# Optimization experiments

Measured on AMD Instinct MI355X. Metric: run time of the kernel, lower is better.

The kernel has to match this reference:

```python
import jax, jax.numpy as jnp
import numpy as np

B, L, R, D = 64, 512, 512, 512
F_CONV, H = 100, 60

def setup_inputs() -> dict:
    key = jax.random.key(0)
    ks = jax.random.split(key, 8)
    l_lengths = jax.random.randint(ks[0], (B,), L // 2, L + 1)
    r_lengths = jax.random.randint(ks[1], (B,), R // 2, R + 1)
    l_vectors = jax.random.normal(ks[2], (L, B, D), jnp.float32)
    r_vectors = jax.random.normal(ks[3], (R, B, D), jnp.float32)
    Wconv = jax.random.normal(ks[4], (F_CONV, D), jnp.float32) / np.sqrt(D).astype(np.float32)
    bconv = jnp.zeros((F_CONV,), jnp.float32)
    Wd = jax.random.normal(ks[5], (H, 2 * F_CONV), jnp.float32) / np.sqrt(2 * F_CONV).astype(np.float32)
    bd = jnp.zeros((H,), jnp.float32)
    return {"l_lengths": l_lengths, "l_vectors": l_vectors, "r_lengths": r_lengths,
            "r_vectors": r_vectors, "Wconv": Wconv, "bconv": bconv, "Wd": Wd, "bd": bd}

def reference(l_lengths, l_vectors, r_lengths, r_vectors, Wconv, bconv, Wd, bd):
    Lm, Bm, Dm = l_vectors.shape
    Rm = r_vectors.shape[0]
    # masks, seq-first [L,B] like pad_sequence output
    l_mask = (jnp.arange(Lm)[:, None] < l_lengths[None, :]).astype(l_vectors.dtype)
    r_mask = (jnp.arange(Rm)[:, None] < r_lengths[None, :]).astype(r_vectors.dtype)
    lmT, rmT = l_mask.T, r_mask.T  # [B,L], [B,R]

    # co-attention scores [B,L,R]
    attention = jnp.einsum('lbd,rbd->blr', l_vectors, r_vectors)
    attention = attention * lmT[:, :, None] * rmT[:, None, :]

    att_r = jax.nn.softmax(attention - 10.0 * (1.0 - lmT[:, :, None]), axis=1)
    att_r = att_r * lmT[:, :, None]
    att_r = att_r / (att_r.sum(axis=1, keepdims=True) + 1e-13)

    att_l = jax.nn.softmax(attention - 10.0 * (1.0 - rmT[:, None, :]), axis=2)
    att_l = att_l * rmT[:, None, :]
    att_l = att_l / (att_l.sum(axis=2, keepdims=True) + 1e-13)

    # ---- left side: stats + top-1 hard attention ----
    rl = r_lengths.astype(l_vectors.dtype)[:, None]
    l_mean = att_l.sum(axis=2) / rl                              # [B,L]
    l_w = (att_l * att_l).sum(axis=2) / rl - l_mean * l_mean
    l_w = l_w / jnp.maximum(l_mean, 0.001)
    l_a = att_l.max(axis=2)                                      # top-1 value [B,L]
    l_i = att_l.argmax(axis=2)                                   # top-1 index [B,L]
    l_i = l_i * lmT.astype(l_i.dtype)
    l_a = l_a / jnp.maximum(l_a, 0.001)                          # k=1: sum == value
    gathered = jnp.take_along_axis(r_vectors, l_i.T[:, :, None], axis=0)  # [L,B,D]
    l_counter = l_a.T[:, :, None] * gathered
    l_c = l_w.T[:, :, None] * jnp.abs(l_vectors - l_counter) * l_mask[:, :, None]

    # ---- right side ----
    ll = l_lengths.astype(r_vectors.dtype)[:, None]
    r_mean = att_r.sum(axis=1) / ll                              # [B,R]
    r_w = (att_r * att_r).sum(axis=1) / ll - r_mean * r_mean
    r_w = r_w / jnp.maximum(r_mean, 0.001)
    r_a = att_r.max(axis=1)                                      # [B,R]
    r_i = att_r.argmax(axis=1)
    r_i = r_i * rmT.astype(r_i.dtype)
    r_a = r_a / jnp.maximum(r_a, 0.001)
    gathered_r = jnp.take_along_axis(l_vectors, r_i.T[:, :, None], axis=0)  # [R,B,D]
    r_counter = r_a.T[:, :, None] * gathered_r
    r_c = r_w.T[:, :, None] * jnp.abs(r_vectors - r_counter) * r_mask[:, :, None]

    # SentenceConv(1, 100, dim): kernel (1, dim) conv == per-position linear,
    # ReLU, masked max-pool over the sequence.
    def sconv(x, mask):  # x [S,B,D], mask [S,B]
        h = jax.nn.relu(jnp.einsum('sbd,fd->bsf', x, Wconv) + bconv)  # [B,S,F]
        h = h - (1.0 - mask.T)[:, :, None] * 1e9
        return h.max(axis=1)  # [B,F]

    feats = jnp.concatenate([sconv(l_c, l_mask), sconv(r_c, r_mask)], axis=1)  # [B,200]
    return jax.nn.relu(feats @ Wd.T + bd)  # [B,60]
```

## Files before the change

kernel.cpp:

```cpp
#include <hip/hip_runtime.h>
#include <math.h>

#define BB 64
#define LL 512
#define RR 512
#define DD 512
#define FC 100
#define FP 112
#define HH 60
#define BD (BB*DD)

typedef __attribute__((ext_vector_type(8))) short bf16x8;
typedef __attribute__((ext_vector_type(4))) float f32x4;

__device__ __forceinline__ unsigned short bf16rne(float x) {
  unsigned u = __float_as_uint(x);
  return (unsigned short)((u + 0x7fffu + ((u >> 16) & 1u)) >> 16);
}
__device__ __forceinline__ float bf16tof(unsigned short h) {
  return __uint_as_float((unsigned)h << 16);
}

__device__ __forceinline__ void bar_lgkm() {
  asm volatile("s_waitcnt lgkmcnt(0)" ::: "memory");
  __builtin_amdgcn_s_barrier();
}

__device__ __forceinline__ void split2(float x0, float x1, unsigned& h2, unsigned& l2) {
  unsigned u0 = __float_as_uint(x0), u1 = __float_as_uint(x1);
  h2 = __builtin_amdgcn_perm(u1, u0, 0x07060302u);
  float r0 = x0 - __uint_as_float(u0 & 0xffff0000u);
  float r1 = x1 - __uint_as_float(u1 & 0xffff0000u);
  l2 = __builtin_amdgcn_perm(__float_as_uint(r1), __float_as_uint(r0), 0x07060302u);
}

template <int N>
__device__ __forceinline__ float ror_max_f(float v) {
  return fmaxf(v, __uint_as_float(__builtin_amdgcn_mov_dpp(__float_as_uint(v), 0x120 | N, 0xf, 0xf, true)));
}
template <int N>
__device__ __forceinline__ float ror_add_f(float v) {
  return v + __uint_as_float(__builtin_amdgcn_mov_dpp(__float_as_uint(v), 0x120 | N, 0xf, 0xf, true));
}
template <int N>
__device__ __forceinline__ int ror_min_i(int v) {
  int o = __builtin_amdgcn_mov_dpp(v, 0x120 | N, 0xf, 0xf, true);
  return o < v ? o : v;
}
__device__ __forceinline__ float row16_max(float v) {
  v = ror_max_f<1>(v); v = ror_max_f<2>(v); v = ror_max_f<4>(v); return ror_max_f<8>(v);
}
__device__ __forceinline__ float row16_sum(float v) {
  v = ror_add_f<1>(v); v = ror_add_f<2>(v); v = ror_add_f<4>(v); return ror_add_f<8>(v);
}
__device__ __forceinline__ int row16_min(int v) {
  v = ror_min_i<1>(v); v = ror_min_i<2>(v); v = ror_min_i<4>(v); return ror_min_i<8>(v);
}

__global__ __launch_bounds__(512, 2) void gemm_att(const float* __restrict__ lv,
                                                   const float* __restrict__ rv,
                                                   const int* __restrict__ llen,
                                                   const int* __restrict__ rlen,
                                                   float4* __restrict__ lpart,
                                                   float4* __restrict__ rpart) {
  __shared__ __align__(16) unsigned short Ah[2][256][32];
  __shared__ __align__(16) unsigned short Al[2][256][32];
  __shared__ __align__(16) unsigned short Bh[2][256][32];
  __shared__ __align__(16) unsigned short Bl[2][256][32];

  const int bid = blockIdx.x;
  const int wid = (bid & 7) * 32 + (bid >> 3);
  const int b  = wid >> 2;
  const int l0 = ((wid >> 1) & 1) * 256;
  const int r0 = (wid & 1) * 256;

  const int t = threadIdx.x;
  const int srow = t >> 1;
  const int half = t & 1;

  const float* Abase = lv + (size_t)(l0 + srow) * BD + b * DD + half * 16;
  const float* Bbase = rv + (size_t)(r0 + srow) * BD + b * DD + half * 16;

  const int sl0 = (((2 * half) ^ ((srow >> 1) & 3)) * 8);
  const int sl1 = (((2 * half + 1) ^ ((srow >> 1) & 3)) * 8);

  const int lane = t & 63;
  const int wv = t >> 6;
  const int wrow = wv >> 2;
  const int wcol = wv & 3;
  const int fr = lane & 15;
  const int kh = lane >> 4;
  const int koff = (kh ^ ((fr >> 1) & 3)) * 8;

  float4 pa[4], pb[4];

#define LOADCHUNK(n) { const int cn_ = ((n) < 15 ? (n) : 15) * 32; \
    const float* An = Abase + cn_; const float* Bn = Bbase + cn_; \
    pa[0] = *(const float4*)(An);     pa[1] = *(const float4*)(An + 4); \
    pa[2] = *(const float4*)(An + 8); pa[3] = *(const float4*)(An + 12); \
    pb[0] = *(const float4*)(Bn);     pb[1] = *(const float4*)(Bn + 4); \
    pb[2] = *(const float4*)(Bn + 8); pb[3] = *(const float4*)(Bn + 12); }

#define STAGE(nb) { unsigned h01, l01, h23, l23, h45, l45, h67, l67; \
    split2(pa[0].x, pa[0].y, h01, l01); split2(pa[0].z, pa[0].w, h23, l23); \
    split2(pa[1].x, pa[1].y, h45, l45); split2(pa[1].z, pa[1].w, h67, l67); \
    *(uint4*)&Ah[nb][srow][sl0] = make_uint4(h01, h23, h45, h67); \
    *(uint4*)&Al[nb][srow][sl0] = make_uint4(l01, l23, l45, l67); \
    split2(pa[2].x, pa[2].y, h01, l01); split2(pa[2].z, pa[2].w, h23, l23); \
    split2(pa[3].x, pa[3].y, h45, l45); split2(pa[3].z, pa[3].w, h67, l67); \
    *(uint4*)&Ah[nb][srow][sl1] = make_uint4(h01, h23, h45, h67); \
    *(uint4*)&Al[nb][srow][sl1] = make_uint4(l01, l23, l45, l67); \
    split2(pb[0].x, pb[0].y, h01, l01); split2(pb[0].z, pb[0].w, h23, l23); \
    split2(pb[1].x, pb[1].y, h45, l45); split2(pb[1].z, pb[1].w, h67, l67); \
    *(uint4*)&Bh[nb][srow][sl0] = make_uint4(h01, h23, h45, h67); \
    *(uint4*)&Bl[nb][srow][sl0] = make_uint4(l01, l23, l45, l67); \
    split2(pb[2].x, pb[2].y, h01, l01); split2(pb[2].z, pb[2].w, h23, l23); \
    split2(pb[3].x, pb[3].y, h45, l45); split2(pb[3].z, pb[3].w, h67, l67); \
    *(uint4*)&Bh[nb][srow][sl1] = make_uint4(h01, h23, h45, h67); \
    *(uint4*)&Bl[nb][srow][sl1] = make_uint4(l01, l23, l45, l67); }

#define COMPUTE(cb) { bf16x8 bh4[4], bl4[4]; \
    _Pragma("unroll") \
    for (int j = 0; j < 4; ++j) { \
      bh4[j] = *(const bf16x8*)&Bh[cb][wcol * 64 + j * 16 + fr][koff]; \
      bl4[j] = *(const bf16x8*)&Bl[cb][wcol * 64 + j * 16 + fr][koff]; \
    } \
    __builtin_amdgcn_s_setprio(1); \
    _Pragma("unroll") \
    for (int i = 0; i < 8; ++i) { \
      bf16x8 a_h = *(const bf16x8*)&Ah[cb][wrow * 128 + i * 16 + fr][koff]; \
      bf16x8 a_l = *(const bf16x8*)&Al[cb][wrow * 128 + i * 16 + fr][koff]; \
      _Pragma("unroll") \
      for (int j = 0; j < 4; ++j) { \
        acc[i][j] = __builtin_amdgcn_mfma_f32_16x16x32_bf16(a_h, bh4[j], acc[i][j], 0, 0, 0); \
        acc[i][j] = __builtin_amdgcn_mfma_f32_16x16x32_bf16(a_h, bl4[j], acc[i][j], 0, 0, 0); \
        acc[i][j] = __builtin_amdgcn_mfma_f32_16x16x32_bf16(a_l, bh4[j], acc[i][j], 0, 0, 0); \
      } \
    } \
    __builtin_amdgcn_s_setprio(0); }

  f32x4 acc[8][4];
#pragma unroll
  for (int i = 0; i < 8; ++i)
#pragma unroll
    for (int j = 0; j < 4; ++j) acc[i][j] = (f32x4){0.f, 0.f, 0.f, 0.f};

  LOADCHUNK(0);
  STAGE(0);
  LOADCHUNK(1);
  bar_lgkm();

  for (int p2 = 0; p2 < 8; ++p2) {
    const int c = p2 * 2;
    STAGE(1);
    LOADCHUNK(c + 2);
    COMPUTE(0);
    bar_lgkm();
    STAGE(0);
    LOADCHUNK(c + 3);
    COMPUTE(1);
    bar_lgkm();
  }

  const int ll_ = llen[b], rl_ = rlen[b];
  __syncthreads();
  float4* rowsc = (float4*)&Ah[0][0][0];
  float4* colsc = (float4*)&Bh[0][0][0];

  const int rbase = r0 + wcol * 64 + fr;
  bool vr4[4]; int rr4[4];
#pragma unroll
  for (int j = 0; j < 4; ++j) { rr4[j] = rbase + j * 16; vr4[j] = rr4[j] < rl_; }

#pragma unroll
  for (int i = 0; i < 8; ++i) {
#pragma unroll
    for (int q = 0; q < 4; ++q) {
      const int trow = wrow * 128 + i * 16 + kh * 4 + q;
      const bool vl = (l0 + trow) < ll_;
      float s[4];
      float M = -1e30f;
#pragma unroll
      for (int j = 0; j < 4; ++j) {
        float raw = acc[i][j][q];
        s[j] = !vr4[j] ? -10.f : (vl ? raw : 0.f);
        M = fmaxf(M, s[j]);
      }
      M = row16_max(M);
      float zv = 0.f, q2 = 0.f;
      int loc = 0x7fffffff;
#pragma unroll
      for (int j = 0; j < 4; ++j) {
        float e = __expf(s[j] - M);
        if (vr4[j]) {
          zv += e; q2 += e * e;
          if (s[j] == M && rr4[j] < loc) loc = rr4[j];
        }
      }
      zv = row16_sum(zv);
      q2 = row16_sum(q2);
      loc = row16_min(loc);
      if (fr == 0)
        rowsc[wcol * 256 + trow] = make_float4(M, zv, q2, __int_as_float(loc));
    }
  }

#pragma unroll
  for (int j = 0; j < 4; ++j) {
    const int tcol = wcol * 64 + j * 16 + fr;
    const bool vr = (r0 + tcol) < rl_;
    float M = -1e30f;
#pragma unroll
    for (int i = 0; i < 8; ++i)
#pragma unroll
      for (int q = 0; q < 4; ++q) {
        int lg = l0 + wrow * 128 + i * 16 + kh * 4 + q;
        bool vl = lg < ll_;
        float sv = !vl ? -10.f : (vr ? acc[i][j][q] : 0.f);
        M = fmaxf(M, sv);
      }
    M = fmaxf(M, __shfl_xor(M, 16, 64));
    M = fmaxf(M, __shfl_xor(M, 32, 64));
    float zv = 0.f, q2 = 0.f;
    int loc = 0x7fffffff;
#pragma unroll
    for (int i = 0; i < 8; ++i)
#pragma unroll
      for (int q = 0; q < 4; ++q) {
        int lg = l0 + wrow * 128 + i * 16 + kh * 4 + q;
        bool vl = lg < ll_;
        float sv = !vl ? -10.f : (vr ? acc[i][j][q] : 0.f);
        float e = __expf(sv - M);
        if (vl) {
          zv += e; q2 += e * e;
          if (sv == M && lg < loc) loc = lg;
        }
      }
    zv += __shfl_xor(zv, 16, 64); zv += __shfl_xor(zv, 32, 64);
    q2 += __shfl_xor(q2, 16, 64); q2 += __shfl_xor(q2, 32, 64);
    { int o = __shfl_xor(loc, 16, 64); loc = o < loc ? o : loc; }
    { int o = __shfl_xor(loc, 32, 64); loc = o < loc ? o : loc; }
    if (kh == 0)
      colsc[wrow * 256 + tcol] = make_float4(M, zv, q2, __int_as_float(loc));
  }

  __syncthreads();

  if (t < 256) {
    float4 p = rowsc[t];
    float M = p.x, zv = p.y, q2 = p.z;
    int loc = __float_as_int(p.w);
#pragma unroll
    for (int w2 = 1; w2 < 4; ++w2) {
      float4 o = rowsc[w2 * 256 + t];
      float M1 = o.x;
      float Mn = fmaxf(M, M1);
      float c0 = __expf(M - Mn), c1 = __expf(M1 - Mn);
      zv = zv * c0 + o.y * c1;
      q2 = q2 * c0 * c0 + o.z * c1 * c1;
      int loc1 = __float_as_int(o.w);
      loc = (M1 > M) ? loc1 : ((M1 == M && loc1 < loc) ? loc1 : loc);
      M = Mn;
    }
    lpart[((size_t)(b * 512 + l0 + t)) * 2 + (r0 >> 8)] =
        make_float4(M, zv, q2, __int_as_float(loc));
  } else {
    const int c = t - 256;
    float4 p = colsc[c];
    float M = p.x, zv = p.y, q2 = p.z;
    int loc = __float_as_int(p.w);
    {
      float4 o = colsc[256 + c];
      float M1 = o.x;
      float Mn = fmaxf(M, M1);
      float c0 = __expf(M - Mn), c1 = __expf(M1 - Mn);
      zv = zv * c0 + o.y * c1;
      q2 = q2 * c0 * c0 + o.z * c1 * c1;
      int loc1 = __float_as_int(o.w);
      loc = (M1 > M) ? loc1 : ((M1 == M && loc1 < loc) ? loc1 : loc);
      M = Mn;
    }
    rpart[((size_t)(b * 512 + r0 + c)) * 2 + (l0 >> 8)] =
        make_float4(M, zv, q2, __int_as_float(loc));
  }
#undef LOADCHUNK
#undef STAGE
#undef COMPUTE
}

__global__ __launch_bounds__(256) void stats_merge(const float4* __restrict__ lpart,
    const float4* __restrict__ rpart,
    const int* __restrict__ llen, const int* __restrict__ rlen,
    float* __restrict__ lwv, float* __restrict__ lan, int* __restrict__ lidx,
    float* __restrict__ rwv, float* __restrict__ ran, int* __restrict__ ridx) {
  const int gid = blockIdx.x * 256 + threadIdx.x;
  const int side = gid >> 15;
  const int pos = gid & 32767;
  const int b = pos >> 9, p = pos & 511;
  const float4* part = (side ? rpart : lpart) + (size_t)pos * 2;
  float4 P0 = part[0], P1 = part[1];
  float M = P0.x, zv = P0.y, q2 = P0.z;
  int loc = __float_as_int(P0.w);
  {
    float M1 = P1.x;
    float Mn = fmaxf(M, M1);
    float c0 = __expf(M - Mn), c1 = __expf(M1 - Mn);
    zv = zv * c0 + P1.y * c1;
    q2 = q2 * c0 * c0 + P1.z * c1 * c1;
    int loc1 = __float_as_int(P1.w);
    loc = (M1 > M) ? loc1 : ((M1 == M && loc1 < loc) ? loc1 : loc);
    M = Mn;
  }
  const int len = side ? llen[b] : rlen[b];
  const int own = side ? rlen[b] : llen[b];
  const int ninv = side ? (LL - llen[b]) : (RR - rlen[b]);
  float z0 = zv + (float)ninv * __expf(-10.f - M);
  float S = zv / z0;
  float inv = 1.f / (S + 1e-13f);
  float sumq = S * inv;
  float mean = sumq / (float)len;
  float sumq2 = q2 / (z0 * z0) * inv * inv;
  float var = sumq2 / (float)len - mean * mean;
  float wv = var / fmaxf(mean, 0.001f);
  float qmax = inv / z0;
  float an = qmax / fmaxf(qmax, 0.001f);
  int idx = (p < own && loc != 0x7fffffff) ? loc : 0;
  if (side == 0) { lwv[pos] = wv; lan[pos] = an; lidx[pos] = idx; }
  else           { rwv[pos] = wv; ran[pos] = an; ridx[pos] = idx; }
}

__global__ void prep_w(const float* __restrict__ Wconv,
                       unsigned short* __restrict__ Whg, unsigned short* __restrict__ Wlg) {
  int i = blockIdx.x * 256 + threadIdx.x;
  if (i < FP * DD) {
    int f = i >> 9;
    float w = (f < FC) ? Wconv[i] : 0.f;
    unsigned short h = bf16rne(w);
    unsigned short l = bf16rne(w - bf16tof(h));
    Whg[i] = h; Wlg[i] = l;
  }
}

__global__ __launch_bounds__(256) void conv_pool_mfma(const float* __restrict__ lv,
    const float* __restrict__ rv,
    const float* __restrict__ lwv, const float* __restrict__ lan, const int* __restrict__ lidx,
    const float* __restrict__ rwv, const float* __restrict__ ran, const int* __restrict__ ridx,
    const int* __restrict__ llen, const int* __restrict__ rlen,
    const unsigned short* __restrict__ Whg, const unsigned short* __restrict__ Wlg,
    const float* __restrict__ bconv, float* __restrict__ feat) {
  __shared__ __align__(16) unsigned short Ah[128][40];
  __shared__ __align__(16) unsigned short Al[128][40];
  __shared__ __align__(16) unsigned short Wh[FP][40];
  __shared__ __align__(16) unsigned short Wl[FP][40];
  __shared__ float pool[4][FP];
  __shared__ float ppw[128], ppa[128];
  __shared__ int   ppi[128], ppv[128];

  const int bid = blockIdx.x;
  const int wid = (bid & 7) * 64 + (bid >> 3);
  const int side = wid >> 8;
  const int b    = (wid >> 2) & 63;
  const int s0   = (wid & 3) * 128;

  const int t = threadIdx.x;
  const float* x; const float* y; const float* wb; const float* ab; const int* ib; int plen;
  if (side == 0) { x = lv; y = rv; wb = lwv; ab = lan; ib = lidx; plen = llen[b]; }
  else           { x = rv; y = lv; wb = rwv; ab = ran; ib = ridx; plen = rlen[b]; }

  if (t < 128) {
    int pos = s0 + t;
    ppw[t] = wb[b * 512 + pos];
    ppa[t] = ab[b * 512 + pos];
    ppi[t] = ib[b * 512 + pos];
    ppv[t] = (pos < plen) ? 1 : 0;
  }
  __syncthreads();

  const int pos  = t >> 1;
  const int half = t & 1;
  const float w_ = ppw[pos];
  const float a_ = ppa[pos];
  const int   yi = ppi[pos];
  const float* xp = x + (size_t)(s0 + pos) * BD + b * DD + half * 16;
  const float* yp = y + (size_t)yi * BD + b * DD + half * 16;

  float4 xv[4], yv[4];
#pragma unroll
  for (int q = 0; q < 4; ++q) {
    xv[q] = *(const float4*)(xp + q * 4);
    yv[q] = *(const float4*)(yp + q * 4);
  }

  const int lane = t & 63;
  const int wvi = t >> 6;
  const int m0 = wvi * 32;
  const int fr = lane & 15;
  const int kh = lane >> 4;

  f32x4 acc[2][7];
#pragma unroll
  for (int i = 0; i < 2; ++i)
#pragma unroll
    for (int j = 0; j < 7; ++j) acc[i][j] = (f32x4){0.f, 0.f, 0.f, 0.f};

  for (int it = 0; it < 16; ++it) {
    const int k0 = it * 32;
    __syncthreads();
#pragma unroll
    for (int q = 0; q < 2; ++q) {
      float d0 = w_ * fabsf(xv[2*q].x   - a_ * yv[2*q].x);
      float d1 = w_ * fabsf(xv[2*q].y   - a_ * yv[2*q].y);
      float d2 = w_ * fabsf(xv[2*q].z   - a_ * yv[2*q].z);
      float d3 = w_ * fabsf(xv[2*q].w   - a_ * yv[2*q].w);
      float d4 = w_ * fabsf(xv[2*q+1].x - a_ * yv[2*q+1].x);
      float d5 = w_ * fabsf(xv[2*q+1].y - a_ * yv[2*q+1].y);
      float d6 = w_ * fabsf(xv[2*q+1].z - a_ * yv[2*q+1].z);
      float d7 = w_ * fabsf(xv[2*q+1].w - a_ * yv[2*q+1].w);
      unsigned h01, l01, h23, l23, h45, l45, h67, l67;
      split2(d0, d1, h01, l01);
      split2(d2, d3, h23, l23);
      split2(d4, d5, h45, l45);
      split2(d6, d7, h67, l67);
      *(uint4*)&Ah[pos][half * 16 + q * 8] = make_uint4(h01, h23, h45, h67);
      *(uint4*)&Al[pos][half * 16 + q * 8] = make_uint4(l01, l23, l45, l67);
    }
#pragma unroll
    for (int rep = 0; rep < 2; ++rep) {
      int idx = t + rep * 256;
      if (idx < FP * 4) {
        int f = idx >> 2, q = idx & 3;
        *(ulonglong2*)&Wh[f][q * 8] = *(const ulonglong2*)&Whg[f * DD + k0 + q * 8];
        *(ulonglong2*)&Wl[f][q * 8] = *(const ulonglong2*)&Wlg[f * DD + k0 + q * 8];
      }
    }
    if (it < 15) {
      const float* xn = xp + k0 + 32;
      const float* yn = yp + k0 + 32;
#pragma unroll
      for (int q = 0; q < 4; ++q) {
        xv[q] = *(const float4*)(xn + q * 4);
        yv[q] = *(const float4*)(yn + q * 4);
      }
    }
    __syncthreads();

    bf16x8 ah[2], al[2];
#pragma unroll
    for (int i = 0; i < 2; ++i) {
      ah[i] = *(const bf16x8*)&Ah[m0 + i * 16 + fr][kh * 8];
      al[i] = *(const bf16x8*)&Al[m0 + i * 16 + fr][kh * 8];
    }
#pragma unroll
    for (int j = 0; j < 7; ++j) {
      bf16x8 bh = *(const bf16x8*)&Wh[j * 16 + fr][kh * 8];
      bf16x8 bl = *(const bf16x8*)&Wl[j * 16 + fr][kh * 8];
#pragma unroll
      for (int i = 0; i < 2; ++i) {
        acc[i][j] = __builtin_amdgcn_mfma_f32_16x16x32_bf16(ah[i], bh, acc[i][j], 0, 0, 0);
        acc[i][j] = __builtin_amdgcn_mfma_f32_16x16x32_bf16(ah[i], bl, acc[i][j], 0, 0, 0);
        acc[i][j] = __builtin_amdgcn_mfma_f32_16x16x32_bf16(al[i], bh, acc[i][j], 0, 0, 0);
      }
    }
  }

#pragma unroll
  for (int j = 0; j < 7; ++j) {
    int f = j * 16 + fr;
    float bcv = (f < FC) ? bconv[f] : 0.f;
    float vmax = -1e30f;
#pragma unroll
    for (int i = 0; i < 2; ++i) {
#pragma unroll
      for (int q = 0; q < 4; ++q) {
        int sl = m0 + i * 16 + kh * 4 + q;
        if (ppv[sl]) vmax = fmaxf(vmax, fmaxf(acc[i][j][q] + bcv, 0.f));
      }
    }
    vmax = fmaxf(vmax, __shfl_xor(vmax, 16, 64));
    vmax = fmaxf(vmax, __shfl_xor(vmax, 32, 64));
    if (lane < 16) pool[wvi][f] = vmax;
  }
  __syncthreads();
  if (t < FC) {
    float v = fmaxf(fmaxf(pool[0][t], pool[1][t]), fmaxf(pool[2][t], pool[3][t]));
    if (v > -1e29f) atomicMax((int*)&feat[b * 200 + side * FC + t], __float_as_int(v));
  }
}

__global__ void dense_out(const float* __restrict__ feat, const float* __restrict__ Wd,
                          const float* __restrict__ bd, float* __restrict__ out) {
  int b = blockIdx.x, h = threadIdx.x;
  if (h < HH) {
    float s = bd[h];
    const float* fb = feat + b * 200;
    const float* wr = Wd + h * 200;
    for (int k = 0; k < 200; ++k) s += fb[k] * wr[k];
    out[b * HH + h] = fmaxf(s, 0.f);
  }
}

extern "C" void kernel_launch(void* const* d_in, const int* in_sizes, int n_in,
                              void* d_out, int out_size, void* d_ws, size_t ws_size,
                              hipStream_t stream) {
  (void)in_sizes; (void)n_in; (void)out_size; (void)ws_size;
  const int*   llen  = (const int*)d_in[0];
  const float* lv    = (const float*)d_in[1];
  const int*   rlen  = (const int*)d_in[2];
  const float* rv    = (const float*)d_in[3];
  const float* Wconv = (const float*)d_in[4];
  const float* bconv = (const float*)d_in[5];
  const float* Wd    = (const float*)d_in[6];
  const float* bd    = (const float*)d_in[7];
  float* out = (float*)d_out;
  char* ws = (char*)d_ws;
  size_t off = 0;
  unsigned short* Whg = (unsigned short*)(ws + off); off += (size_t)FP * DD * 2;
  unsigned short* Wlg = (unsigned short*)(ws + off); off += (size_t)FP * DD * 2;
  float4* lpart = (float4*)(ws + off); off += (size_t)BB * LL * 2 * 16;
  float4* rpart = (float4*)(ws + off); off += (size_t)BB * RR * 2 * 16;
  float* lwv = (float*)(ws + off); off += (size_t)BB * LL * 4;
  float* lan = (float*)(ws + off); off += (size_t)BB * LL * 4;
  int*   lidx= (int*)  (ws + off); off += (size_t)BB * LL * 4;
  float* rwv = (float*)(ws + off); off += (size_t)BB * RR * 4;
  float* ran = (float*)(ws + off); off += (size_t)BB * RR * 4;
  int*   ridx= (int*)  (ws + off); off += (size_t)BB * RR * 4;
  float* feat= (float*)(ws + off); off += (size_t)BB * 200 * 4;

  hipMemsetAsync(feat, 0, BB * 200 * 4, stream);
  prep_w<<<(FP * DD + 255) / 256, 256, 0, stream>>>(Wconv, Whg, Wlg);
  gemm_att<<<dim3(256), 512, 0, stream>>>(lv, rv, llen, rlen, lpart, rpart);
  stats_merge<<<dim3(256), 256, 0, stream>>>(lpart, rpart, llen, rlen,
                                             lwv, lan, lidx, rwv, ran, ridx);
  conv_pool_mfma<<<dim3(512), 256, 0, stream>>>(lv, rv, lwv, lan, lidx,
                                                rwv, ran, ridx, llen, rlen,
                                                Whg, Wlg, bconv, feat);
  dense_out<<<BB, 64, 0, stream>>>(feat, Wd, bd, out);
}
```

Measured before the change: 115.3 us.

## Double-buffer LDS tiles in conv_pool_mfma with XOR swizzle and one barrier per step

The conv/pool MFMA kernel is restructured to double-buffer its A and W tiles in shared memory. The next tile is staged while the current one is multiplied, so each k-step needs a single barrier instead of two. The padded 40-wide rows become 32-wide rows with an XOR swizzle to avoid bank conflicts, and s_setprio raises priority around the MFMA block. Launch bounds now request 2 blocks per CU. The risks are higher register pressure, the correctness of the custom bar_lgkm barrier, and the redundant final-iteration loads that are clamped to tile 15.

```diff
diff --git a/kernel.cpp b/kernel.cpp
--- a/kernel.cpp
+++ b/kernel.cpp
@@ -341,17 +341,17 @@
   }
 }
 
-__global__ __launch_bounds__(256) void conv_pool_mfma(const float* __restrict__ lv,
+__global__ __launch_bounds__(256, 2) void conv_pool_mfma(const float* __restrict__ lv,
     const float* __restrict__ rv,
     const float* __restrict__ lwv, const float* __restrict__ lan, const int* __restrict__ lidx,
     const float* __restrict__ rwv, const float* __restrict__ ran, const int* __restrict__ ridx,
     const int* __restrict__ llen, const int* __restrict__ rlen,
     const unsigned short* __restrict__ Whg, const unsigned short* __restrict__ Wlg,
     const float* __restrict__ bconv, float* __restrict__ feat) {
-  __shared__ __align__(16) unsigned short Ah[128][40];
-  __shared__ __align__(16) unsigned short Al[128][40];
-  __shared__ __align__(16) unsigned short Wh[FP][40];
-  __shared__ __align__(16) unsigned short Wl[FP][40];
+  __shared__ __align__(16) unsigned short Ah[2][128][32];
+  __shared__ __align__(16) unsigned short Al[2][128][32];
+  __shared__ __align__(16) unsigned short Wh[2][FP][32];
+  __shared__ __align__(16) unsigned short Wl[2][FP][32];
   __shared__ float pool[4][FP];
   __shared__ float ppw[128], ppa[128];
   __shared__ int   ppi[128], ppv[128];
@@ -384,18 +384,87 @@
   const float* xp = x + (size_t)(s0 + pos) * BD + b * DD + half * 16;
   const float* yp = y + (size_t)yi * BD + b * DD + half * 16;
 
-  float4 xv[4], yv[4];
-#pragma unroll
-  for (int q = 0; q < 4; ++q) {
-    xv[q] = *(const float4*)(xp + q * 4);
-    yv[q] = *(const float4*)(yp + q * 4);
-  }
+  const int asl0 = (((2 * half) ^ ((pos >> 1) & 3)) * 8);
+  const int asl1 = (((2 * half + 1) ^ ((pos >> 1) & 3)) * 8);
+
+  const int idx1 = (t < 192) ? t + 256 : t;
+  const int f0 = t >> 2,   q0 = t & 3;
+  const int f1 = idx1 >> 2, q1 = idx1 & 3;
+  const int wsl0 = ((q0 ^ ((f0 >> 1) & 3)) * 8);
+  const int wsl1 = ((q1 ^ ((f1 >> 1) & 3)) * 8);
 
   const int lane = t & 63;
   const int wvi = t >> 6;
   const int m0 = wvi * 32;
   const int fr = lane & 15;
   const int kh = lane >> 4;
+  const int koff = (kh ^ ((fr >> 1) & 3)) * 8;
+
+  float4 xv[4], yv[4];
+  uint4 w0h, w0l, w1h, w1l;
+
+#define LOADX(n) { const int off = ((n) < 15 ? (n) : 15) * 32; \
+    xv[0] = *(const float4*)(xp + off);      xv[1] = *(const float4*)(xp + off + 4); \
+    xv[2] = *(const float4*)(xp + off + 8);  xv[3] = *(const float4*)(xp + off + 12); \
+    yv[0] = *(const float4*)(yp + off);      yv[1] = *(const float4*)(yp + off + 4); \
+    yv[2] = *(const float4*)(yp + off + 8);  yv[3] = *(const float4*)(yp + off + 12); }
+
+#define LOADW(n) { const int off = ((n) < 15 ? (n) : 15) * 32; \
+    w0h = *(const uint4*)&Whg[f0 * DD + off + q0 * 8]; \
+    w0l = *(const uint4*)&Wlg[f0 * DD + off + q0 * 8]; \
+    w1h = *(const uint4*)&Whg[f1 * DD + off + q1 * 8]; \
+    w1l = *(const uint4*)&Wlg[f1 * DD + off + q1 * 8]; }
+
+#define STAGEA(nb) { \
+    float d0 = w_ * fabsf(xv[0].x - a_ * yv[0].x); \
+    float d1 = w_ * fabsf(xv[0].y - a_ * yv[0].y); \
+    float d2 = w_ * fabsf(xv[0].z - a_ * yv[0].z); \
+    float d3 = w_ * fabsf(xv[0].w - a_ * yv[0].w); \
+    float d4 = w_ * fabsf(xv[1].x - a_ * yv[1].x); \
+    float d5 = w_ * fabsf(xv[1].y - a_ * yv[1].y); \
+    float d6 = w_ * fabsf(xv[1].z - a_ * yv[1].z); \
+    float d7 = w_ * fabsf(xv[1].w - a_ * yv[1].w); \
+    unsigned h01, l01, h23, l23, h45, l45, h67, l67; \
+    split2(d0, d1, h01, l01); split2(d2, d3, h23, l23); \
+    split2(d4, d5, h45, l45); split2(d6, d7, h67, l67); \
+    *(uint4*)&Ah[nb][pos][asl0] = make_uint4(h01, h23, h45, h67); \
+    *(uint4*)&Al[nb][pos][asl0] = make_uint4(l01, l23, l45, l67); \
+    d0 = w_ * fabsf(xv[2].x - a_ * yv[2].x); \
+    d1 = w_ * fabsf(xv[2].y - a_ * yv[2].y); \
+    d2 = w_ * fabsf(xv[2].z - a_ * yv[2].z); \
+    d3 = w_ * fabsf(xv[2].w - a_ * yv[2].w); \
+    d4 = w_ * fabsf(xv[3].x - a_ * yv[3].x); \
+    d5 = w_ * fabsf(xv[3].y - a_ * yv[3].y); \
+    d6 = w_ * fabsf(xv[3].z - a_ * yv[3].z); \
+    d7 = w_ * fabsf(xv[3].w - a_ * yv[3].w); \
+    split2(d0, d1, h01, l01); split2(d2, d3, h23, l23); \
+    split2(d4, d5, h45, l45); split2(d6, d7, h67, l67); \
+    *(uint4*)&Ah[nb][pos][asl1] = make_uint4(h01, h23, h45, h67); \
+    *(uint4*)&Al[nb][pos][asl1] = make_uint4(l01, l23, l45, l67); }
+
+#define STAGEW(nb) { \
+    *(uint4*)&Wh[nb][f0][wsl0] = w0h; *(uint4*)&Wl[nb][f0][wsl0] = w0l; \
+    *(uint4*)&Wh[nb][f1][wsl1] = w1h; *(uint4*)&Wl[nb][f1][wsl1] = w1l; }
+
+#define COMPUTEC(cb) { bf16x8 ah[2], al[2]; \
+    _Pragma("unroll") \
+    for (int i = 0; i < 2; ++i) { \
+      ah[i] = *(const bf16x8*)&Ah[cb][m0 + i * 16 + fr][koff]; \
+      al[i] = *(const bf16x8*)&Al[cb][m0 + i * 16 + fr][koff]; \
+    } \
+    __builtin_amdgcn_s_setprio(1); \
+    _Pragma("unroll") \
+    for (int j = 0; j < 7; ++j) { \
+      bf16x8 bh = *(const bf16x8*)&Wh[cb][j * 16 + fr][koff]; \
+      bf16x8 bl = *(const bf16x8*)&Wl[cb][j * 16 + fr][koff]; \
+      _Pragma("unroll") \
+      for (int i = 0; i < 2; ++i) { \
+        acc[i][j] = __builtin_amdgcn_mfma_f32_16x16x32_bf16(ah[i], bh, acc[i][j], 0, 0, 0); \
+        acc[i][j] = __builtin_amdgcn_mfma_f32_16x16x32_bf16(ah[i], bl, acc[i][j], 0, 0, 0); \
+        acc[i][j] = __builtin_amdgcn_mfma_f32_16x16x32_bf16(al[i], bh, acc[i][j], 0, 0, 0); \
+      } \
+    } \
+    __builtin_amdgcn_s_setprio(0); }
 
   f32x4 acc[2][7];
 #pragma unroll
@@ -403,64 +472,21 @@
 #pragma unroll
     for (int j = 0; j < 7; ++j) acc[i][j] = (f32x4){0.f, 0.f, 0.f, 0.f};
 
-  for (int it = 0; it < 16; ++it) {
-    const int k0 = it * 32;
-    __syncthreads();
-#pragma unroll
-    for (int q = 0; q < 2; ++q) {
-      float d0 = w_ * fabsf(xv[2*q].x   - a_ * yv[2*q].x);
-      float d1 = w_ * fabsf(xv[2*q].y   - a_ * yv[2*q].y);
-      float d2 = w_ * fabsf(xv[2*q].z   - a_ * yv[2*q].z);
-      float d3 = w_ * fabsf(xv[2*q].w   - a_ * yv[2*q].w);
-      float d4 = w_ * fabsf(xv[2*q+1].x - a_ * yv[2*q+1].x);
-      float d5 = w_ * fabsf(xv[2*q+1].y - a_ * yv[2*q+1].y);
-      float d6 = w_ * fabsf(xv[2*q+1].z - a_ * yv[2*q+1].z);
-      float d7 = w_ * fabsf(xv[2*q+1].w - a_ * yv[2*q+1].w);
-      unsigned h01, l01, h23, l23, h45, l45, h67, l67;
-      split2(d0, d1, h01, l01);
-      split2(d2, d3, h23, l23);
-      split2(d4, d5, h45, l45);
-      split2(d6, d7, h67, l67);
-      *(uint4*)&Ah[pos][half * 16 + q * 8] = make_uint4(h01, h23, h45, h67);
-      *(uint4*)&Al[pos][half * 16 + q * 8] = make_uint4(l01, l23, l45, l67);
-    }
-#pragma unroll
-    for (int rep = 0; rep < 2; ++rep) {
-      int idx = t + rep * 256;
-      if (idx < FP * 4) {
-        int f = idx >> 2, q = idx & 3;
-        *(ulonglong2*)&Wh[f][q * 8] = *(const ulonglong2*)&Whg[f * DD + k0 + q * 8];
-        *(ulonglong2*)&Wl[f][q * 8] = *(const ulonglong2*)&Wlg[f * DD + k0 + q * 8];
-      }
-    }
-    if (it < 15) {
-      const float* xn = xp + k0 + 32;
-      const float* yn = yp + k0 + 32;
-#pragma unroll
-      for (int q = 0; q < 4; ++q) {
-        xv[q] = *(const float4*)(xn + q * 4);
-        yv[q] = *(const float4*)(yn + q * 4);
-      }
-    }
-    __syncthreads();
-
-    bf16x8 ah[2], al[2];
-#pragma unroll
-    for (int i = 0; i < 2; ++i) {
-      ah[i] = *(const bf16x8*)&Ah[m0 + i * 16 + fr][kh * 8];
-      al[i] = *(const bf16x8*)&Al[m0 + i * 16 + fr][kh * 8];
-    }
-#pragma unroll
-    for (int j = 0; j < 7; ++j) {
-      bf16x8 bh = *(const bf16x8*)&Wh[j * 16 + fr][kh * 8];
-      bf16x8 bl = *(const bf16x8*)&Wl[j * 16 + fr][kh * 8];
-#pragma unroll
-      for (int i = 0; i < 2; ++i) {
-        acc[i][j] = __builtin_amdgcn_mfma_f32_16x16x32_bf16(ah[i], bh, acc[i][j], 0, 0, 0);
-        acc[i][j] = __builtin_amdgcn_mfma_f32_16x16x32_bf16(ah[i], bl, acc[i][j], 0, 0, 0);
-        acc[i][j] = __builtin_amdgcn_mfma_f32_16x16x32_bf16(al[i], bh, acc[i][j], 0, 0, 0);
-      }
-    }
+  LOADX(0); LOADW(0);
+  STAGEA(0); STAGEW(0);
+  LOADX(1); LOADW(1);
+  bar_lgkm();
+
+  for (int p2 = 0; p2 < 8; ++p2) {
+    const int c = p2 * 2;
+    STAGEA(1); STAGEW(1);
+    LOADX(c + 2); LOADW(c + 2);
+    COMPUTEC(0);
+    bar_lgkm();
+    STAGEA(0); STAGEW(0);
+    LOADX(c + 3); LOADW(c + 3);
+    COMPUTEC(1);
+    bar_lgkm();
   }
 
 #pragma unroll
@@ -485,6 +511,11 @@
     float v = fmaxf(fmaxf(pool[0][t], pool[1][t]), fmaxf(pool[2][t], pool[3][t]));
     if (v > -1e29f) atomicMax((int*)&feat[b * 200 + side * FC + t], __float_as_int(v));
   }
+#undef LOADX
+#undef LOADW
+#undef STAGEA
+#undef STAGEW
+#undef COMPUTEC
 }
 
 __global__ void dense_out(const float* __restrict__ feat, const float* __restrict__ Wd,
```

New measurement: 116.4 us. Within noise of the previous version (+1.0%).
